# Performance work log

Hardware: AMD Instinct MI355X
Metric: run time of the kernel (lower is better)

Reference implementation:

```python
import jax, jax.numpy as jnp
import numpy as np

ALPHA = 0.2  # leaky-relu negative slope
NEG_INF = -9e15


def setup_inputs() -> dict:
    key = jax.random.key(0)
    ks = jax.random.split(key, 10)
    bz, N, Fin, Fout = 16, 1024, 1024, 1024
    h = jax.random.normal(ks[0], (bz, N, Fin), dtype=jnp.float32)
    h_xReact = jax.random.normal(ks[1], (bz, N, Fout), dtype=jnp.float32)
    h_oReact = jax.random.normal(ks[2], (bz, N, Fout), dtype=jnp.float32)
    utt_xReact_mask = (jax.random.uniform(ks[3], (bz, N, N)) > 0.5).astype(jnp.float32)
    utt_oReact_mask = (jax.random.uniform(ks[4], (bz, N, N)) > 0.5).astype(jnp.float32)
    W = jax.random.normal(ks[5], (Fin, Fout), dtype=jnp.float32) * 0.02
    a_SS = jax.random.normal(ks[6], (2 * Fout, 1), dtype=jnp.float32) * 0.05
    a_DS = jax.random.normal(ks[7], (2 * Fout, 1), dtype=jnp.float32) * 0.05
    csk_W = jax.random.normal(ks[8], (Fout, Fout), dtype=jnp.float32) * 0.02
    csk_b = jnp.zeros((Fout,), dtype=jnp.float32)
    return {"h": h, "h_xReact": h_xReact, "h_oReact": h_oReact,
            "utt_xReact_mask": utt_xReact_mask, "utt_oReact_mask": utt_oReact_mask,
            "W": W, "a_SS": a_SS, "a_DS": a_DS, "csk_W": csk_W, "csk_b": csk_b}


def _scores(Wh, h_react, a, mask):
    # e[b,i,j] = leaky_relu(Wh[b,i].a1 + (Wh[b,j]+h_react[b,j]).a2) * mask[b,i,j]
    F = Wh.shape[-1]
    a1, a2 = a[:F, 0], a[F:, 0]
    s_src = Wh @ a1                      # [bz, N]
    s_dst = (Wh + h_react) @ a2          # [bz, N]
    e = jax.nn.leaky_relu(s_src[:, :, None] + s_dst[:, None, :], negative_slope=ALPHA)
    return e * mask


def reference(h, h_xReact, h_oReact, utt_xReact_mask, utt_oReact_mask,
              W, a_SS, a_DS, csk_W, csk_b):
    Wh = h @ W                                       # [bz, N, F]
    hx = h_xReact @ csk_W.T + csk_b                  # csk_linear
    ho = h_oReact @ csk_W.T + csk_b
    e_SS = _scores(Wh, hx, a_SS, utt_xReact_mask)    # [bz, N, N]
    e_DS = _scores(Wh, ho, a_DS, utt_oReact_mask)
    e = e_SS + e_DS
    # faithful to source bug: adj uses xReact mask twice
    adj = utt_xReact_mask + utt_xReact_mask
    att = jax.nn.softmax(jnp.where(adj > 0, e, NEG_INF), axis=-1)
    # dropout: eval mode (deterministic reference) -> identity
    h_prime = att @ Wh                               # [bz, N, F]
    return jax.nn.elu(h_prime)                       # concat=True
```

## Files before the change

### kernel.cpp

```cpp
#include <hip/hip_runtime.h>
#include <hip/hip_bf16.h>
#include <math.h>

#define BZ 16
#define NN 1024
#define FF 1024
#define ALPHA 0.2f
#define NEG_INF (-9e15f)

typedef __bf16 bf16x8 __attribute__((ext_vector_type(8)));
typedef __bf16 bf16x4 __attribute__((ext_vector_type(4)));
typedef float  f32x4  __attribute__((ext_vector_type(4)));

#define GLOBAL_AS __attribute__((address_space(1)))
#define LDS_AS    __attribute__((address_space(3)))

__device__ inline void load_lds16(const void* g, void* l) {
    __builtin_amdgcn_global_load_lds((const GLOBAL_AS void*)g, (LDS_AS void*)l, 16, 0, 0);
}

__device__ inline float waveReduceSum(float v) {
    for (int o = 32; o; o >>= 1) v += __shfl_down(v, o);
    return v;
}
__device__ inline float waveReduceMax(float v) {
    for (int o = 32; o; o >>= 1) v = fmaxf(v, __shfl_down(v, o));
    return v;
}

template<int EPI>
__global__ __launch_bounds__(512, 2) void gemm256(
    const __bf16* __restrict__ A, const __bf16* __restrict__ Bt,
    float* __restrict__ Cf, __bf16* __restrict__ Ct, size_t sB)
{
    __shared__ char lds[131072];

    const int bid = blockIdx.x;
    const int l   = (bid & 7) * 32 + (bid >> 3);
    const int tileM = (l >> 2) * 256;
    const int tileN = (l & 3) * 256;

    const int tid = threadIdx.x, lane = tid & 63, wid = tid >> 6;
    const int wr = wid >> 2, wc = wid & 3;

    const int batch = tileM >> 10;
    const char* Ab  = (const char*)(A + (size_t)tileM * FF);
    const char* Bbp = (const char*)(Bt + (size_t)batch * sB + (size_t)tileN * FF);

    const int o1 = wid * 1024 + lane * 16;
    const int o2 = o1 + 8192;
    const int r1 = o1 >> 7, r2 = o2 >> 7;
    const size_t raoff1 = (size_t)r1 * 2048 + ((o1 & 127) ^ ((r1 & 7) << 4));
    const size_t raoff2 = (size_t)r2 * 2048 + ((o2 & 127) ^ ((r2 & 7) << 4));

#define STAGE(gb, ldsoff, half, kt) do {                                        \
    const char* g_ = (gb) + (size_t)(half) * (128 * 2048) + (size_t)(kt) * 128; \
    load_lds16(g_ + raoff1, lds + (ldsoff) + (half) * 16384 + wid * 1024);      \
    load_lds16(g_ + raoff2, lds + (ldsoff) + (half) * 16384 + 8192 + wid * 1024);\
} while (0)

    const int fr = lane & 15, kq = lane >> 4;
    const int fswz = (fr & 7) << 4;
    const int ck0 = (kq * 16) ^ fswz;
    const int ck1 = (64 + kq * 16) ^ fswz;
    const int abase = (wr * 128 + fr) * 128;
    const int bbase = 32768 + (wc * 64 + fr) * 128;

#define RD(off) (*(const bf16x8*)(lds + (off)))
#define DSA(P, f0) do { _Pragma("unroll") for (int m = 0; m < 4; ++m) {      \
    av[m][0] = RD((P) * 65536 + abase + (f0 + m) * 2048 + ck0);              \
    av[m][1] = RD((P) * 65536 + abase + (f0 + m) * 2048 + ck1); } } while (0)
#define DSB(P, f0, bv_) do { _Pragma("unroll") for (int n = 0; n < 2; ++n) { \
    bv_[n][0] = RD((P) * 65536 + bbase + (f0 + n) * 2048 + ck0);             \
    bv_[n][1] = RD((P) * 65536 + bbase + (f0 + n) * 2048 + ck1); } } while (0)
#define MFMAQ(m0, bv_, n0) do {                                              \
    _Pragma("unroll") for (int m = 0; m < 4; ++m)                            \
    _Pragma("unroll") for (int n = 0; n < 2; ++n) {                          \
        acc[m0 + m][n0 + n] = __builtin_amdgcn_mfma_f32_16x16x32_bf16(       \
            av[m][0], bv_[n][0], acc[m0 + m][n0 + n], 0, 0, 0);              \
        acc[m0 + m][n0 + n] = __builtin_amdgcn_mfma_f32_16x16x32_bf16(       \
            av[m][1], bv_[n][1], acc[m0 + m][n0 + n], 0, 0, 0); } } while (0)
#define BAR   __builtin_amdgcn_s_barrier()
#define LGKM0 do { asm volatile("s_waitcnt lgkmcnt(0)" ::: "memory");        \
                   __builtin_amdgcn_sched_barrier(0); } while (0)
#define VM4   asm volatile("s_waitcnt vmcnt(4)" ::: "memory")
#define VM0   asm volatile("s_waitcnt vmcnt(0)" ::: "memory")
#define PRIO1 __builtin_amdgcn_s_setprio(1)
#define PRIO0 __builtin_amdgcn_s_setprio(0)

    f32x4 acc[8][4];
    #pragma unroll
    for (int m = 0; m < 8; ++m)
        #pragma unroll
        for (int n = 0; n < 4; ++n) acc[m][n] = (f32x4){0.f, 0.f, 0.f, 0.f};

    bf16x8 av[4][2], bvL[2][2], bvH[2][2];

    STAGE(Ab,      0, 0, 0);  STAGE(Ab,      0, 1, 0);
    STAGE(Bbp, 32768, 0, 0);  STAGE(Bbp, 32768, 1, 0);
    STAGE(Bbp, 65536 + 32768, 0, 1);
    STAGE(Ab,  65536,         0, 1);
    VM4; BAR;

    const int NT = FF / 64;
    for (int it = 0; it < NT / 2; ++it) {
        const int t   = 2 * it;
        const int kt1 = t + 1;
        const int kt2 = (t + 2 < NT) ? t + 2 : NT - 1;
        const int kt3 = (t + 3 < NT) ? t + 3 : NT - 1;

        DSA(0, 0); DSB(0, 0, bvL);
        STAGE(Ab, 65536, 1, kt1);
        BAR; LGKM0; PRIO1; MFMAQ(0, bvL, 0); PRIO0; BAR;
        DSB(0, 2, bvH);
        STAGE(Bbp, 65536 + 32768, 1, kt1);
        BAR; LGKM0; PRIO1; MFMAQ(0, bvH, 2); PRIO0; BAR;
        DSA(0, 4);
        STAGE(Bbp, 32768, 0, kt2);
        BAR; LGKM0; PRIO1; MFMAQ(4, bvL, 0); PRIO0; BAR;
        STAGE(Ab, 0, 0, kt2);
        BAR; PRIO1; MFMAQ(4, bvH, 2); PRIO0; VM4; BAR;

        DSA(1, 0); DSB(1, 0, bvL);
        STAGE(Ab, 0, 1, kt2);
        BAR; LGKM0; PRIO1; MFMAQ(0, bvL, 0); PRIO0; BAR;
        DSB(1, 2, bvH);
        STAGE(Bbp, 32768, 1, kt2);
        BAR; LGKM0; PRIO1; MFMAQ(0, bvH, 2); PRIO0; BAR;
        DSA(1, 4);
        STAGE(Bbp, 65536 + 32768, 0, kt3);
        BAR; LGKM0; PRIO1; MFMAQ(4, bvL, 0); PRIO0; BAR;
        STAGE(Ab, 65536, 0, kt3);
        BAR; PRIO1; MFMAQ(4, bvH, 2); PRIO0; VM4; BAR;
    }

    if (EPI == 1) {
        #pragma unroll
        for (int fm = 0; fm < 8; ++fm) {
            const int row0 = tileM + wr * 128 + fm * 16 + kq * 4;
            #pragma unroll
            for (int fn = 0; fn < 4; ++fn) {
                const int col = tileN + wc * 64 + fn * 16 + fr;
                #pragma unroll
                for (int r = 0; r < 4; ++r) {
                    float v = acc[fm][fn][r];
                    v = (v > 0.f) ? v : expm1f(v);
                    Cf[(size_t)(row0 + r) * FF + col] = v;
                }
            }
        }
    } else {
        VM0; BAR;
        char* wlds = lds + wid * 16384;
        #pragma unroll
        for (int fm = 0; fm < 8; ++fm)
            #pragma unroll
            for (int fn = 0; fn < 4; ++fn) {
                const int ccol = fn * 16 + fr;
                const int crow = fm * 16 + kq * 4;
                int addr = (ccol * 256 + crow * 2) ^ ((ccol & 7) << 4);
                bf16x4 v = { (__bf16)acc[fm][fn][0], (__bf16)acc[fm][fn][1],
                             (__bf16)acc[fm][fn][2], (__bf16)acc[fm][fn][3] };
                *(bf16x4*)(wlds + addr) = v;
            }
        const int jb = (tileM & 1023) + wr * 128;
        __bf16* Wt = Ct + (size_t)batch * (1024 * 1024);
        #pragma unroll
        for (int pass = 0; pass < 16; ++pass) {
            const int fl  = pass * 4 + (lane >> 4);
            const int jby = (lane & 15) * 16;
            int addr = (fl * 256 + jby) ^ ((fl & 7) << 4);
            bf16x8 v = *(const bf16x8*)(wlds + addr);
            const int fg = tileN + wc * 64 + fl;
            *(bf16x8*)((char*)(Wt + (size_t)fg * 1024 + jb) + jby) = v;
        }
    }
#undef STAGE
#undef RD
#undef DSA
#undef DSB
#undef MFMAQ
}

__global__ __launch_bounds__(256) void cvt_bf16(
    const float* __restrict__ in, __bf16* __restrict__ out, size_t n8)
{
    size_t t = (size_t)blockIdx.x * 256 + threadIdx.x;
    if (t >= n8) return;
    const float4* i4 = (const float4*)in;
    float4 a = i4[t * 2], b = i4[t * 2 + 1];
    bf16x8 v = { (__bf16)a.x, (__bf16)a.y, (__bf16)a.z, (__bf16)a.w,
                 (__bf16)b.x, (__bf16)b.y, (__bf16)b.z, (__bf16)b.w };
    ((bf16x8*)out)[t] = v;
}

__global__ __launch_bounds__(256) void transpose_cvt(
    const float* __restrict__ in, __bf16* __restrict__ out, int R, int C)
{
    const float* ib = in;
    __bf16* ob = out;
    const int r0 = blockIdx.y * 64;
    const int c0 = blockIdx.x * 64;
    __shared__ __bf16 t[64][66];
    #pragma unroll
    for (int it = 0; it < 16; ++it) {
        int idx = threadIdx.x + it * 256;
        int r = idx >> 6, c = idx & 63;
        t[r][c] = (__bf16)ib[(size_t)(r0 + r) * C + c0 + c];
    }
    __syncthreads();
    #pragma unroll
    for (int it = 0; it < 4; ++it) {
        int idx = threadIdx.x + it * 256;
        int rr = idx >> 4;
        int cc = (idx & 15) * 4;
        bf16x4 v = { t[cc][rr], t[cc + 1][rr], t[cc + 2][rr], t[cc + 3][rr] };
        *(bf16x4*)&ob[(size_t)(c0 + rr) * R + r0 + cc] = v;
    }
}

__global__ __launch_bounds__(256) void prep_wa(
    const float* __restrict__ W, const float* __restrict__ aSS,
    const float* __restrict__ aDS, float* __restrict__ wa)
{
    const int i = blockIdx.x;
    const int t = threadIdx.x;
    float4 w  = ((const float4*)(W + (size_t)i * FF))[t];
    float4 s1 = ((const float4*)aSS)[t];
    float4 s2 = ((const float4*)(aSS + FF))[t];
    float4 d1 = ((const float4*)aDS)[t];
    float4 d2 = ((const float4*)(aDS + FF))[t];
    float v0 = w.x * s1.x + w.y * s1.y + w.z * s1.z + w.w * s1.w;
    float v1 = w.x * s2.x + w.y * s2.y + w.z * s2.z + w.w * s2.w;
    float v2 = w.x * d1.x + w.y * d1.y + w.z * d1.z + w.w * d1.w;
    float v3 = w.x * d2.x + w.y * d2.y + w.z * d2.z + w.w * d2.w;
    v0 = waveReduceSum(v0); v1 = waveReduceSum(v1);
    v2 = waveReduceSum(v2); v3 = waveReduceSum(v3);
    __shared__ float red[4][4];
    int wid = t >> 6;
    if ((t & 63) == 0) { red[wid][0] = v0; red[wid][1] = v1; red[wid][2] = v2; red[wid][3] = v3; }
    __syncthreads();
    if (t < 4) {
        float s = red[0][t] + red[1][t] + red[2][t] + red[3][t];
        wa[(size_t)t * FF + i] = s;
    }
}

__global__ __launch_bounds__(256) void prep_v(
    const float* __restrict__ cskW, const float* __restrict__ aSS,
    const float* __restrict__ aDS, float* __restrict__ vSS, float* __restrict__ vDS)
{
    const int g0 = blockIdx.x * 64;
    const int gl = threadIdx.x & 63;
    const int fs = threadIdx.x >> 6;
    const int g = g0 + gl;
    float aS = 0.f, aD = 0.f;
    for (int f = fs * 256; f < fs * 256 + 256; ++f) {
        float w = cskW[(size_t)f * FF + g];
        aS += w * aSS[FF + f];
        aD += w * aDS[FF + f];
    }
    __shared__ float rS[4][64], rD[4][64];
    rS[fs][gl] = aS; rD[fs][gl] = aD;
    __syncthreads();
    if (fs == 0) {
        vSS[g] = rS[0][gl] + rS[1][gl] + rS[2][gl] + rS[3][gl];
        vDS[g] = rD[0][gl] + rD[1][gl] + rD[2][gl] + rD[3][gl];
    }
}

__global__ __launch_bounds__(256) void prep_c(
    const float* __restrict__ cskb, const float* __restrict__ aSS,
    const float* __restrict__ aDS, float* __restrict__ cv)
{
    int t = threadIdx.x;
    float cS = 0.f, cD = 0.f;
    for (int f = t; f < FF; f += 256) {
        float bb = cskb[f];
        cS += bb * aSS[FF + f];
        cD += bb * aDS[FF + f];
    }
    cS = waveReduceSum(cS);
    cD = waveReduceSum(cD);
    __shared__ float rA[4], rB[4];
    int wid = t >> 6;
    if ((t & 63) == 0) { rA[wid] = cS; rB[wid] = cD; }
    __syncthreads();
    if (t == 0) {
        cv[0] = rA[0] + rA[1] + rA[2] + rA[3];
        cv[1] = rB[0] + rB[1] + rB[2] + rB[3];
    }
}

__global__ __launch_bounds__(256) void row_scores2(
    const float* __restrict__ h, const float* __restrict__ hx, const float* __restrict__ ho,
    const float* __restrict__ wa, const float* __restrict__ vSS, const float* __restrict__ vDS,
    const float* __restrict__ cv,
    float* __restrict__ sSrcSS, float* __restrict__ sDstSS,
    float* __restrict__ sSrcDS, float* __restrict__ sDstDS)
{
    const int row = blockIdx.x;
    const int t = threadIdx.x;
    float4 hv = ((const float4*)(h  + (size_t)row * FF))[t];
    float4 xv = ((const float4*)(hx + (size_t)row * FF))[t];
    float4 ov = ((const float4*)(ho + (size_t)row * FF))[t];
    float4 w0 = ((const float4*)wa)[t];
    float4 w1 = ((const float4*)(wa + FF))[t];
    float4 w2 = ((const float4*)(wa + 2 * FF))[t];
    float4 w3 = ((const float4*)(wa + 3 * FF))[t];
    float4 vs = ((const float4*)vSS)[t];
    float4 vd = ((const float4*)vDS)[t];
    float d0 = hv.x * w0.x + hv.y * w0.y + hv.z * w0.z + hv.w * w0.w;
    float d1 = hv.x * w1.x + hv.y * w1.y + hv.z * w1.z + hv.w * w1.w;
    float d2 = hv.x * w2.x + hv.y * w2.y + hv.z * w2.z + hv.w * w2.w;
    float d3 = hv.x * w3.x + hv.y * w3.y + hv.z * w3.z + hv.w * w3.w;
    float d4 = xv.x * vs.x + xv.y * vs.y + xv.z * vs.z + xv.w * vs.w;
    float d5 = ov.x * vd.x + ov.y * vd.y + ov.z * vd.z + ov.w * vd.w;
    d0 = waveReduceSum(d0); d1 = waveReduceSum(d1); d2 = waveReduceSum(d2);
    d3 = waveReduceSum(d3); d4 = waveReduceSum(d4); d5 = waveReduceSum(d5);
    __shared__ float red[4][6];
    int wid = t >> 6;
    if ((t & 63) == 0) {
        red[wid][0] = d0; red[wid][1] = d1; red[wid][2] = d2;
        red[wid][3] = d3; red[wid][4] = d4; red[wid][5] = d5;
    }
    __syncthreads();
    if (t == 0) {
        float s0 = 0, s1 = 0, s2 = 0, s3 = 0, s4 = 0, s5 = 0;
        for (int w = 0; w < 4; ++w) {
            s0 += red[w][0]; s1 += red[w][1]; s2 += red[w][2];
            s3 += red[w][3]; s4 += red[w][4]; s5 += red[w][5];
        }
        sSrcSS[row] = s0;
        sDstSS[row] = s1 + s4 + cv[0];
        sSrcDS[row] = s2;
        sDstDS[row] = s3 + s5 + cv[1];
    }
}

__global__ __launch_bounds__(256) void softmax_att(
    const float* __restrict__ mx, const float* __restrict__ mo,
    const float* __restrict__ sSrcSS, const float* __restrict__ sDstSS,
    const float* __restrict__ sSrcDS, const float* __restrict__ sDstDS,
    __bf16* __restrict__ att)
{
    const int row = blockIdx.x;
    const int base = row & ~(NN - 1);
    const int t = threadIdx.x;
    const float srcS = sSrcSS[row];
    const float srcD = sSrcDS[row];
    const float4* mxr = (const float4*)(mx + (size_t)row * NN);
    const float4* mor = (const float4*)(mo + (size_t)row * NN);
    const float4* dSp = (const float4*)(sDstSS + base);
    const float4* dDp = (const float4*)(sDstDS + base);

    float4 a = mxr[t], o = mor[t], dS = dSp[t], dD = dDp[t];
    const float* ap = (const float*)&a;
    const float* op = (const float*)&o;
    const float* sp = (const float*)&dS;
    const float* dp = (const float*)&dD;

    float ev[4];
    float m = -INFINITY;
    #pragma unroll
    for (int l = 0; l < 4; ++l) {
        float eS = srcS + sp[l];
        float lS = (eS >= 0.f) ? eS : ALPHA * eS;
        float eD = srcD + dp[l];
        float lD = (eD >= 0.f) ? eD : ALPHA * eD;
        float val = (ap[l] > 0.f) ? (lS * ap[l] + lD * op[l]) : NEG_INF;
        ev[l] = val;
        m = fmaxf(m, val);
    }
    m = waveReduceMax(m);
    __shared__ float redA[4], redB[4];
    int wid = t >> 6;
    if ((t & 63) == 0) redA[wid] = m;
    __syncthreads();
    float bm = fmaxf(fmaxf(redA[0], redA[1]), fmaxf(redA[2], redA[3]));

    float s = 0.f;
    #pragma unroll
    for (int l = 0; l < 4; ++l) {
        float p = expf(ev[l] - bm);
        ev[l] = p;
        s += p;
    }
    s = waveReduceSum(s);
    if ((t & 63) == 0) redB[wid] = s;
    __syncthreads();
    float bs = redB[0] + redB[1] + redB[2] + redB[3];
    float inv = 1.f / bs;

    bf16x4 v = { (__bf16)(ev[0] * inv), (__bf16)(ev[1] * inv),
                 (__bf16)(ev[2] * inv), (__bf16)(ev[3] * inv) };
    *(bf16x4*)&att[(size_t)row * NN + t * 4] = v;
}

extern "C" void kernel_launch(void* const* d_in, const int* in_sizes, int n_in,
                              void* d_out, int out_size, void* d_ws, size_t ws_size,
                              hipStream_t stream)
{
    const float* h    = (const float*)d_in[0];
    const float* hx   = (const float*)d_in[1];
    const float* ho   = (const float*)d_in[2];
    const float* mx   = (const float*)d_in[3];
    const float* mo   = (const float*)d_in[4];
    const float* W    = (const float*)d_in[5];
    const float* aSS  = (const float*)d_in[6];
    const float* aDS  = (const float*)d_in[7];
    const float* cskW = (const float*)d_in[8];
    const float* cskb = (const float*)d_in[9];
    float* out = (float*)d_out;

    char* ws = (char*)d_ws;
    const size_t MB = 1024 * 1024;
    __bf16* h_bf   = (__bf16*)ws;
    __bf16* WhT_bf = (__bf16*)(ws + 32 * MB);
    __bf16* att_bf = (__bf16*)(ws + 64 * MB);
    __bf16* WbfT   = (__bf16*)(ws + 96 * MB);
    float* wa     = (float*)(ws + 98 * MB);
    float* vSS    = wa + 4 * FF;
    float* vDS    = vSS + FF;
    float* cv     = vDS + FF;
    float* sSrcSS = cv + 64;
    float* sDstSS = sSrcSS + BZ * NN;
    float* sSrcDS = sDstSS + BZ * NN;
    float* sDstDS = sSrcDS + BZ * NN;

    const size_t BIG = (size_t)BZ * NN * FF;

    cvt_bf16<<<(int)((BIG / 8 + 255) / 256), 256, 0, stream>>>(h, h_bf, BIG / 8);
    transpose_cvt<<<dim3(16, 16, 1), 256, 0, stream>>>(W, WbfT, FF, FF);
    prep_wa<<<FF, 256, 0, stream>>>(W, aSS, aDS, wa);
    prep_v<<<16, 256, 0, stream>>>(cskW, aSS, aDS, vSS, vDS);
    prep_c<<<1, 256, 0, stream>>>(cskb, aSS, aDS, cv);
    row_scores2<<<BZ * NN, 256, 0, stream>>>(h, hx, ho, wa, vSS, vDS, cv,
                                             sSrcSS, sDstSS, sSrcDS, sDstDS);
    gemm256<2><<<256, 512, 0, stream>>>(h_bf, WbfT, nullptr, WhT_bf, 0);
    softmax_att<<<BZ * NN, 256, 0, stream>>>(mx, mo, sSrcSS, sDstSS, sSrcDS, sDstDS,
                                             att_bf);
    gemm256<1><<<256, 512, 0, stream>>>(att_bf, WhT_bf, out, nullptr,
                                        (size_t)NN * FF);
}
```

Baseline: 209.4 us.

## Fuse h bf16 conversion into row-score kernel and restructure GEMM k-half MFMA order

```diff
diff --git a/kernel.cpp b/kernel.cpp
--- a/kernel.cpp
+++ b/kernel.cpp
@@ -61,25 +61,18 @@
 
     const int fr = lane & 15, kq = lane >> 4;
     const int fswz = (fr & 7) << 4;
-    const int ck0 = (kq * 16) ^ fswz;
-    const int ck1 = (64 + kq * 16) ^ fswz;
+    const int ck[2] = { (kq * 16) ^ fswz, (64 + kq * 16) ^ fswz };
     const int abase = (wr * 128 + fr) * 128;
     const int bbase = 32768 + (wc * 64 + fr) * 128;
 
 #define RD(off) (*(const bf16x8*)(lds + (off)))
-#define DSA(P, f0) do { _Pragma("unroll") for (int m = 0; m < 4; ++m) {      \
-    av[m][0] = RD((P) * 65536 + abase + (f0 + m) * 2048 + ck0);              \
-    av[m][1] = RD((P) * 65536 + abase + (f0 + m) * 2048 + ck1); } } while (0)
-#define DSB(P, f0, bv_) do { _Pragma("unroll") for (int n = 0; n < 2; ++n) { \
-    bv_[n][0] = RD((P) * 65536 + bbase + (f0 + n) * 2048 + ck0);             \
-    bv_[n][1] = RD((P) * 65536 + bbase + (f0 + n) * 2048 + ck1); } } while (0)
-#define MFMAQ(m0, bv_, n0) do {                                              \
+#define RDA(P, m, kh) RD((P) * 65536 + abase + (m) * 2048 + ck[kh])
+#define RDB(P, n, kh) RD((P) * 65536 + bbase + (n) * 2048 + ck[kh])
+#define MF16(amr, bvr, m0) do {                                              \
+    _Pragma("unroll") for (int n = 0; n < 4; ++n)                            \
     _Pragma("unroll") for (int m = 0; m < 4; ++m)                            \
-    _Pragma("unroll") for (int n = 0; n < 2; ++n) {                          \
-        acc[m0 + m][n0 + n] = __builtin_amdgcn_mfma_f32_16x16x32_bf16(       \
-            av[m][0], bv_[n][0], acc[m0 + m][n0 + n], 0, 0, 0);              \
-        acc[m0 + m][n0 + n] = __builtin_amdgcn_mfma_f32_16x16x32_bf16(       \
-            av[m][1], bv_[n][1], acc[m0 + m][n0 + n], 0, 0, 0); } } while (0)
+        acc[m0 + m][n] = __builtin_amdgcn_mfma_f32_16x16x32_bf16(            \
+            amr[m], bvr[n], acc[m0 + m][n], 0, 0, 0); } while (0)
 #define BAR   __builtin_amdgcn_s_barrier()
 #define LGKM0 do { asm volatile("s_waitcnt lgkmcnt(0)" ::: "memory");        \
                    __builtin_amdgcn_sched_barrier(0); } while (0)
@@ -94,7 +87,7 @@
         #pragma unroll
         for (int n = 0; n < 4; ++n) acc[m][n] = (f32x4){0.f, 0.f, 0.f, 0.f};
 
-    bf16x8 av[4][2], bvL[2][2], bvH[2][2];
+    bf16x8 a0[4], a47k0[4], a47k1[4], b0[4], b1[4];
 
     STAGE(Ab,      0, 0, 0);  STAGE(Ab,      0, 1, 0);
     STAGE(Bbp, 32768, 0, 0);  STAGE(Bbp, 32768, 1, 0);
@@ -109,29 +102,43 @@
         const int kt2 = (t + 2 < NT) ? t + 2 : NT - 1;
         const int kt3 = (t + 3 < NT) ? t + 3 : NT - 1;
 
-        DSA(0, 0); DSB(0, 0, bvL);
+        #pragma unroll
+        for (int m = 0; m < 4; ++m) a0[m] = RDA(0, m, 0);
+        #pragma unroll
+        for (int n = 0; n < 4; ++n) b0[n] = RDB(0, n, 0);
         STAGE(Ab, 65536, 1, kt1);
-        BAR; LGKM0; PRIO1; MFMAQ(0, bvL, 0); PRIO0; BAR;
-        DSB(0, 2, bvH);
+        BAR; LGKM0; PRIO1; MF16(a0, b0, 0); PRIO0; BAR;
+        #pragma unroll
+        for (int m = 0; m < 4; ++m) a0[m] = RDA(0, m, 1);
+        #pragma unroll
+        for (int n = 0; n < 4; ++n) b1[n] = RDB(0, n, 1);
         STAGE(Bbp, 65536 + 32768, 1, kt1);
-        BAR; LGKM0; PRIO1; MFMAQ(0, bvH, 2); PRIO0; BAR;
-        DSA(0, 4);
+        BAR; LGKM0; PRIO1; MF16(a0, b1, 0); PRIO0; BAR;
+        #pragma unroll
+        for (int m = 0; m < 4; ++m) { a47k0[m] = RDA(0, 4 + m, 0); a47k1[m] = RDA(0, 4 + m, 1); }
         STAGE(Bbp, 32768, 0, kt2);
-        BAR; LGKM0; PRIO1; MFMAQ(4, bvL, 0); PRIO0; BAR;
+        BAR; LGKM0; PRIO1; MF16(a47k0, b0, 4); PRIO0; BAR;
         STAGE(Ab, 0, 0, kt2);
-        BAR; PRIO1; MFMAQ(4, bvH, 2); PRIO0; VM4; BAR;
-
-        DSA(1, 0); DSB(1, 0, bvL);
+        BAR; PRIO1; MF16(a47k1, b1, 4); PRIO0; VM4; BAR;
+
+        #pragma unroll
+        for (int m = 0; m < 4; ++m) a0[m] = RDA(1, m, 0);
+        #pragma unroll
+        for (int n = 0; n < 4; ++n) b0[n] = RDB(1, n, 0);
         STAGE(Ab, 0, 1, kt2);
-        BAR; LGKM0; PRIO1; MFMAQ(0, bvL, 0); PRIO0; BAR;
-        DSB(1, 2, bvH);
+        BAR; LGKM0; PRIO1; MF16(a0, b0, 0); PRIO0; BAR;
+        #pragma unroll
+        for (int m = 0; m < 4; ++m) a0[m] = RDA(1, m, 1);
+        #pragma unroll
+        for (int n = 0; n < 4; ++n) b1[n] = RDB(1, n, 1);
         STAGE(Bbp, 32768, 1, kt2);
-        BAR; LGKM0; PRIO1; MFMAQ(0, bvH, 2); PRIO0; BAR;
-        DSA(1, 4);
+        BAR; LGKM0; PRIO1; MF16(a0, b1, 0); PRIO0; BAR;
+        #pragma unroll
+        for (int m = 0; m < 4; ++m) { a47k0[m] = RDA(1, 4 + m, 0); a47k1[m] = RDA(1, 4 + m, 1); }
         STAGE(Bbp, 65536 + 32768, 0, kt3);
-        BAR; LGKM0; PRIO1; MFMAQ(4, bvL, 0); PRIO0; BAR;
+        BAR; LGKM0; PRIO1; MF16(a47k0, b0, 4); PRIO0; BAR;
         STAGE(Ab, 65536, 0, kt3);
-        BAR; PRIO1; MFMAQ(4, bvH, 2); PRIO0; VM4; BAR;
+        BAR; PRIO1; MF16(a47k1, b1, 4); PRIO0; VM4; BAR;
     }
 
     if (EPI == 1) {
@@ -177,125 +184,15 @@
     }
 #undef STAGE
 #undef RD
-#undef DSA
-#undef DSB
-#undef MFMAQ
-}
-
-__global__ __launch_bounds__(256) void cvt_bf16(
-    const float* __restrict__ in, __bf16* __restrict__ out, size_t n8)
-{
-    size_t t = (size_t)blockIdx.x * 256 + threadIdx.x;
-    if (t >= n8) return;
-    const float4* i4 = (const float4*)in;
-    float4 a = i4[t * 2], b = i4[t * 2 + 1];
-    bf16x8 v = { (__bf16)a.x, (__bf16)a.y, (__bf16)a.z, (__bf16)a.w,
-                 (__bf16)b.x, (__bf16)b.y, (__bf16)b.z, (__bf16)b.w };
-    ((bf16x8*)out)[t] = v;
-}
-
-__global__ __launch_bounds__(256) void transpose_cvt(
-    const float* __restrict__ in, __bf16* __restrict__ out, int R, int C)
-{
-    const float* ib = in;
-    __bf16* ob = out;
-    const int r0 = blockIdx.y * 64;
-    const int c0 = blockIdx.x * 64;
-    __shared__ __bf16 t[64][66];
-    #pragma unroll
-    for (int it = 0; it < 16; ++it) {
-        int idx = threadIdx.x + it * 256;
-        int r = idx >> 6, c = idx & 63;
-        t[r][c] = (__bf16)ib[(size_t)(r0 + r) * C + c0 + c];
-    }
-    __syncthreads();
-    #pragma unroll
-    for (int it = 0; it < 4; ++it) {
-        int idx = threadIdx.x + it * 256;
-        int rr = idx >> 4;
-        int cc = (idx & 15) * 4;
-        bf16x4 v = { t[cc][rr], t[cc + 1][rr], t[cc + 2][rr], t[cc + 3][rr] };
-        *(bf16x4*)&ob[(size_t)(c0 + rr) * R + r0 + cc] = v;
-    }
-}
-
-__global__ __launch_bounds__(256) void prep_wa(
-    const float* __restrict__ W, const float* __restrict__ aSS,
-    const float* __restrict__ aDS, float* __restrict__ wa)
-{
-    const int i = blockIdx.x;
-    const int t = threadIdx.x;
-    float4 w  = ((const float4*)(W + (size_t)i * FF))[t];
-    float4 s1 = ((const float4*)aSS)[t];
-    float4 s2 = ((const float4*)(aSS + FF))[t];
-    float4 d1 = ((const float4*)aDS)[t];
-    float4 d2 = ((const float4*)(aDS + FF))[t];
-    float v0 = w.x * s1.x + w.y * s1.y + w.z * s1.z + w.w * s1.w;
-    float v1 = w.x * s2.x + w.y * s2.y + w.z * s2.z + w.w * s2.w;
-    float v2 = w.x * d1.x + w.y * d1.y + w.z * d1.z + w.w * d1.w;
-    float v3 = w.x * d2.x + w.y * d2.y + w.z * d2.z + w.w * d2.w;
-    v0 = waveReduceSum(v0); v1 = waveReduceSum(v1);
-    v2 = waveReduceSum(v2); v3 = waveReduceSum(v3);
-    __shared__ float red[4][4];
-    int wid = t >> 6;
-    if ((t & 63) == 0) { red[wid][0] = v0; red[wid][1] = v1; red[wid][2] = v2; red[wid][3] = v3; }
-    __syncthreads();
-    if (t < 4) {
-        float s = red[0][t] + red[1][t] + red[2][t] + red[3][t];
-        wa[(size_t)t * FF + i] = s;
-    }
-}
-
-__global__ __launch_bounds__(256) void prep_v(
-    const float* __restrict__ cskW, const float* __restrict__ aSS,
-    const float* __restrict__ aDS, float* __restrict__ vSS, float* __restrict__ vDS)
-{
-    const int g0 = blockIdx.x * 64;
-    const int gl = threadIdx.x & 63;
-    const int fs = threadIdx.x >> 6;
-    const int g = g0 + gl;
-    float aS = 0.f, aD = 0.f;
-    for (int f = fs * 256; f < fs * 256 + 256; ++f) {
-        float w = cskW[(size_t)f * FF + g];
-        aS += w * aSS[FF + f];
-        aD += w * aDS[FF + f];
-    }
-    __shared__ float rS[4][64], rD[4][64];
-    rS[fs][gl] = aS; rD[fs][gl] = aD;
-    __syncthreads();
-    if (fs == 0) {
-        vSS[g] = rS[0][gl] + rS[1][gl] + rS[2][gl] + rS[3][gl];
-        vDS[g] = rD[0][gl] + rD[1][gl] + rD[2][gl] + rD[3][gl];
-    }
-}
-
-__global__ __launch_bounds__(256) void prep_c(
-    const float* __restrict__ cskb, const float* __restrict__ aSS,
-    const float* __restrict__ aDS, float* __restrict__ cv)
-{
-    int t = threadIdx.x;
-    float cS = 0.f, cD = 0.f;
-    for (int f = t; f < FF; f += 256) {
-        float bb = cskb[f];
-        cS += bb * aSS[FF + f];
-        cD += bb * aDS[FF + f];
-    }
-    cS = waveReduceSum(cS);
-    cD = waveReduceSum(cD);
-    __shared__ float rA[4], rB[4];
-    int wid = t >> 6;
-    if ((t & 63) == 0) { rA[wid] = cS; rB[wid] = cD; }
-    __syncthreads();
-    if (t == 0) {
-        cv[0] = rA[0] + rA[1] + rA[2] + rA[3];
-        cv[1] = rB[0] + rB[1] + rB[2] + rB[3];
-    }
-}
-
-__global__ __launch_bounds__(256) void row_scores2(
+#undef RDA
+#undef RDB
+#undef MF16
+}
+
+__global__ __launch_bounds__(256) void fuse_h(
     const float* __restrict__ h, const float* __restrict__ hx, const float* __restrict__ ho,
     const float* __restrict__ wa, const float* __restrict__ vSS, const float* __restrict__ vDS,
-    const float* __restrict__ cv,
+    const float* __restrict__ cv, __bf16* __restrict__ h_bf,
     float* __restrict__ sSrcSS, float* __restrict__ sDstSS,
     float* __restrict__ sSrcDS, float* __restrict__ sDstDS)
 {
@@ -304,6 +201,10 @@
     float4 hv = ((const float4*)(h  + (size_t)row * FF))[t];
     float4 xv = ((const float4*)(hx + (size_t)row * FF))[t];
     float4 ov = ((const float4*)(ho + (size_t)row * FF))[t];
+
+    bf16x4 hb = { (__bf16)hv.x, (__bf16)hv.y, (__bf16)hv.z, (__bf16)hv.w };
+    *(bf16x4*)&h_bf[(size_t)row * FF + t * 4] = hb;
+
     float4 w0 = ((const float4*)wa)[t];
     float4 w1 = ((const float4*)(wa + FF))[t];
     float4 w2 = ((const float4*)(wa + 2 * FF))[t];
@@ -338,6 +239,104 @@
     }
 }
 
+__global__ __launch_bounds__(256) void transpose_cvt(
+    const float* __restrict__ in, __bf16* __restrict__ out, int R, int C)
+{
+    const float* ib = in;
+    __bf16* ob = out;
+    const int r0 = blockIdx.y * 64;
+    const int c0 = blockIdx.x * 64;
+    __shared__ __bf16 t[64][66];
+    #pragma unroll
+    for (int it = 0; it < 16; ++it) {
+        int idx = threadIdx.x + it * 256;
+        int r = idx >> 6, c = idx & 63;
+        t[r][c] = (__bf16)ib[(size_t)(r0 + r) * C + c0 + c];
+    }
+    __syncthreads();
+    #pragma unroll
+    for (int it = 0; it < 4; ++it) {
+        int idx = threadIdx.x + it * 256;
+        int rr = idx >> 4;
+        int cc = (idx & 15) * 4;
+        bf16x4 v = { t[cc][rr], t[cc + 1][rr], t[cc + 2][rr], t[cc + 3][rr] };
+        *(bf16x4*)&ob[(size_t)(c0 + rr) * R + r0 + cc] = v;
+    }
+}
+
+__global__ __launch_bounds__(256) void prep_wa(
+    const float* __restrict__ W, const float* __restrict__ aSS,
+    const float* __restrict__ aDS, float* __restrict__ wa)
+{
+    const int i = blockIdx.x;
+    const int t = threadIdx.x;
+    float4 w  = ((const float4*)(W + (size_t)i * FF))[t];
+    float4 s1 = ((const float4*)aSS)[t];
+    float4 s2 = ((const float4*)(aSS + FF))[t];
+    float4 d1 = ((const float4*)aDS)[t];
+    float4 d2 = ((const float4*)(aDS + FF))[t];
+    float v0 = w.x * s1.x + w.y * s1.y + w.z * s1.z + w.w * s1.w;
+    float v1 = w.x * s2.x + w.y * s2.y + w.z * s2.z + w.w * s2.w;
+    float v2 = w.x * d1.x + w.y * d1.y + w.z * d1.z + w.w * d1.w;
+    float v3 = w.x * d2.x + w.y * d2.y + w.z * d2.z + w.w * d2.w;
+    v0 = waveReduceSum(v0); v1 = waveReduceSum(v1);
+    v2 = waveReduceSum(v2); v3 = waveReduceSum(v3);
+    __shared__ float red[4][4];
+    int wid = t >> 6;
+    if ((t & 63) == 0) { red[wid][0] = v0; red[wid][1] = v1; red[wid][2] = v2; red[wid][3] = v3; }
+    __syncthreads();
+    if (t < 4) {
+        float s = red[0][t] + red[1][t] + red[2][t] + red[3][t];
+        wa[(size_t)t * FF + i] = s;
+    }
+}
+
+__global__ __launch_bounds__(256) void prep_v(
+    const float* __restrict__ cskW, const float* __restrict__ aSS,
+    const float* __restrict__ aDS, float* __restrict__ vSS, float* __restrict__ vDS)
+{
+    const int g0 = blockIdx.x * 64;
+    const int gl = threadIdx.x & 63;
+    const int fs = threadIdx.x >> 6;
+    const int g = g0 + gl;
+    float aS = 0.f, aD = 0.f;
+    for (int f = fs * 256; f < fs * 256 + 256; ++f) {
+        float w = cskW[(size_t)f * FF + g];
+        aS += w * aSS[FF + f];
+        aD += w * aDS[FF + f];
+    }
+    __shared__ float rS[4][64], rD[4][64];
+    rS[fs][gl] = aS; rD[fs][gl] = aD;
+    __syncthreads();
+    if (fs == 0) {
+        vSS[g] = rS[0][gl] + rS[1][gl] + rS[2][gl] + rS[3][gl];
+        vDS[g] = rD[0][gl] + rD[1][gl] + rD[2][gl] + rD[3][gl];
+    }
+}
+
+__global__ __launch_bounds__(256) void prep_c(
+    const float* __restrict__ cskb, const float* __restrict__ aSS,
+    const float* __restrict__ aDS, float* __restrict__ cv)
+{
+    int t = threadIdx.x;
+    float cS = 0.f, cD = 0.f;
+    for (int f = t; f < FF; f += 256) {
+        float bb = cskb[f];
+        cS += bb * aSS[FF + f];
+        cD += bb * aDS[FF + f];
+    }
+    cS = waveReduceSum(cS);
+    cD = waveReduceSum(cD);
+    __shared__ float rA[4], rB[4];
+    int wid = t >> 6;
+    if ((t & 63) == 0) { rA[wid] = cS; rB[wid] = cD; }
+    __syncthreads();
+    if (t == 0) {
+        cv[0] = rA[0] + rA[1] + rA[2] + rA[3];
+        cv[1] = rB[0] + rB[1] + rB[2] + rB[3];
+    }
+}
+
 __global__ __launch_bounds__(256) void softmax_att(
     const float* __restrict__ mx, const float* __restrict__ mo,
     const float* __restrict__ sSrcSS, const float* __restrict__ sDstSS,
@@ -428,15 +427,12 @@
     float* sSrcDS = sDstSS + BZ * NN;
     float* sDstDS = sSrcDS + BZ * NN;
 
-    const size_t BIG = (size_t)BZ * NN * FF;
-
-    cvt_bf16<<<(int)((BIG / 8 + 255) / 256), 256, 0, stream>>>(h, h_bf, BIG / 8);
-    transpose_cvt<<<dim3(16, 16, 1), 256, 0, stream>>>(W, WbfT, FF, FF);
     prep_wa<<<FF, 256, 0, stream>>>(W, aSS, aDS, wa);
     prep_v<<<16, 256, 0, stream>>>(cskW, aSS, aDS, vSS, vDS);
     prep_c<<<1, 256, 0, stream>>>(cskb, aSS, aDS, cv);
-    row_scores2<<<BZ * NN, 256, 0, stream>>>(h, hx, ho, wa, vSS, vDS, cv,
-                                             sSrcSS, sDstSS, sSrcDS, sDstDS);
+    transpose_cvt<<<dim3(16, 16, 1), 256, 0, stream>>>(W, WbfT, FF, FF);
+    fuse_h<<<BZ * NN, 256, 0, stream>>>(h, hx, ho, wa, vSS, vDS, cv, h_bf,
+                                        sSrcSS, sDstSS, sSrcDS, sDstDS);
     gemm256<2><<<256, 512, 0, stream>>>(h_bf, WbfT, nullptr, WhT_bf, 0);
     softmax_att<<<BZ * NN, 256, 0, stream>>>(mx, mo, sSrcSS, sDstSS, sSrcDS, sDstDS,
                                              att_bf);
```

Measured after the change: 203.7 us. -2.7%, faster.
